# Kernel tuning notes

Hardware: AMD Instinct MI355X
Metric: run time of the kernel (lower is better)

Reference implementation:

```python
import jax, jax.numpy as jnp
import numpy as np

EPS = 1e-6

def setup_inputs() -> dict:
    key = jax.random.key(0)
    k1, k2 = jax.random.split(key)
    patch_feats = jax.random.normal(k1, (576, 768), dtype=jnp.float32)   # [N, D] ViT-B/16 @ 384 -> 24x24 patches
    memory = jax.random.normal(k2, (200000, 768), dtype=jnp.float32)     # [M, D] coreset memory bank
    return {"patch_feats": patch_feats, "memory": memory, "topk": 10}

def reference(patch_feats, memory, topk):
    # L2-normalize both sides (same eps placement as torch: x / (||x|| + eps))
    f = patch_feats / (jnp.linalg.norm(patch_feats, axis=1, keepdims=True) + EPS)  # [N, D]
    m = memory / (jnp.linalg.norm(memory, axis=1, keepdims=True) + EPS)            # [M, D]
    # cosine distance = 1 - sim; min over memory bank. Equivalent to the chunked
    # min-of-mins in the original (min is associative over chunks).
    sim = jnp.einsum('nd,md->nm', f, m)          # [N, M]
    patch_scores = jnp.min(1.0 - sim, axis=1)    # [N]
    # image score: mean of top-k patch scores
    k = min(topk, patch_scores.shape[0])
    topk_vals = jax.lax.top_k(patch_scores, k)[0]
    image_score = jnp.mean(topk_vals)
    return (patch_scores, image_score)
```

## Files before the change

kernel.cpp:

```cpp
#include <hip/hip_runtime.h>
#include <hip/hip_bf16.h>

#define DD 768
#define NPATCH 576
#define NPAD 640
#define NPT 40
#define BMR 64
#define QF 192
#define GRID 256
#define EPSF 1e-6f

typedef short bf16x8 __attribute__((ext_vector_type(8)));
typedef float f32x4 __attribute__((ext_vector_type(4)));

__device__ __forceinline__ unsigned short f2bf(float x) {
  __hip_bfloat16 h = __float2bfloat16(x);
  return __builtin_bit_cast(unsigned short, h);
}

__device__ __forceinline__ void gload_lds16(const float* g, char* lds) {
  __builtin_amdgcn_global_load_lds(
      (const __attribute__((address_space(1))) unsigned int*)(g),
      (__attribute__((address_space(3))) unsigned int*)(lds), 16, 0, 0);
}

__global__ __launch_bounds__(256) void k_norm(const float* __restrict__ pf,
                                              float* __restrict__ invn) {
  int row = blockIdx.x;
  int t = threadIdx.x;
  const float* src = pf + (size_t)row * DD;
  float v0 = src[t], v1 = src[t + 256], v2 = src[t + 512];
  float ss = v0 * v0 + v1 * v1 + v2 * v2;
#pragma unroll
  for (int m = 1; m < 64; m <<= 1) ss += __shfl_xor(ss, m, 64);
  __shared__ float wss[4];
  if ((t & 63) == 0) wss[t >> 6] = ss;
  __syncthreads();
  if (t == 0) {
    float tot = wss[0] + wss[1] + wss[2] + wss[3];
    invn[row] = 1.0f / (sqrtf(tot) + EPSF);
  }
}

__global__ __launch_bounds__(256) void k_pack(const float* __restrict__ pf,
                                              const float* __restrict__ invn,
                                              unsigned short* __restrict__ Fws) {
  int bid = blockIdx.x;
  int ks = bid / NPT, ptg = bid % NPT;
  int t = threadIdx.x;
  int i = t * 2;
  int s = i >> 3, j = i & 7;
  int p = ptg * 16 + (s & 15);
  int k = ks * 32 + (s >> 4) * 8 + j;
  unsigned int outw = 0;
  if (p < NPATCH) {
    float sc = invn[p];
    float a0 = pf[(size_t)p * DD + k] * sc;
    float a1 = pf[(size_t)p * DD + k + 1] * sc;
    outw = (unsigned int)f2bf(a0) | ((unsigned int)f2bf(a1) << 16);
  }
  ((unsigned int*)Fws)[(size_t)bid * 256 + t] = outw;
}

#define PACK_BW(bw, u0, u1)                                               \
  bw.x = (unsigned int)f2bf(u0.x) | ((unsigned int)f2bf(u0.y) << 16);     \
  bw.y = (unsigned int)f2bf(u0.z) | ((unsigned int)f2bf(u0.w) << 16);     \
  bw.z = (unsigned int)f2bf(u1.x) | ((unsigned int)f2bf(u1.y) << 16);     \
  bw.w = (unsigned int)f2bf(u1.z) | ((unsigned int)f2bf(u1.w) << 16);

#define SQ8(u0, u1)                                                        \
  (u0.x * u0.x + u0.y * u0.y + u0.z * u0.z + u0.w * u0.w +                 \
   u1.x * u1.x + u1.y * u1.y + u1.z * u1.z + u1.w * u1.w)

#define STEP(s)                                                              \
  {                                                                          \
    const unsigned short* Ak_ = Abase + (size_t)(q6 + (s)) * (NPT * 512);    \
    bf16x8 a_[5];                                                            \
    _Pragma("unroll") for (int p = 0; p < 5; ++p)                            \
        a_[p] = *(const bf16x8*)(Ak_ + p * 512);                             \
    __builtin_amdgcn_sched_barrier(0);                                       \
    gload_lds16((const float*)(gsrc + sbyte[s]),                             \
                (char*)BsF + dstb + (s) * 8192 + w * 1024);                  \
    __builtin_amdgcn_sched_barrier(0);                                       \
    _Pragma("unroll") for (int rt = 0; rt < 4; ++rt) {                       \
      int o0_ = rt * 12288 + rb768 + ((((s) * 8 + lhi2) ^ sw8x) << 4);       \
      float4 f0_ = *(const float4*)(bp + o0_);                               \
      float4 f1_ = *(const float4*)(bp + (o0_ ^ 16));                        \
      ssr[rt] += SQ8(f0_, f1_);                                              \
      uint4 bw_;                                                             \
      PACK_BW(bw_, f0_, f1_);                                                \
      bf16x8 b_ = __builtin_bit_cast(bf16x8, bw_);                           \
      _Pragma("unroll") for (int p = 0; p < 5; ++p)                          \
        acc[p][rt] = __builtin_amdgcn_mfma_f32_16x16x32_bf16(a_[p], b_, acc[p][rt], 0, 0, 0); \
    }                                                                        \
    __builtin_amdgcn_sched_barrier(0);                                       \
  }

__global__ __launch_bounds__(512, 2) void k_main(const unsigned short* __restrict__ Fws,
                                                 const float* __restrict__ mem,
                                                 float* __restrict__ partial,
                                                 int M, int nchunk) {
  __shared__ __align__(16) float BsF[2][12288];
  __shared__ float ssq[BMR];
  __shared__ float smin[NPAD];

  int t = threadIdx.x;
  int w = t >> 6, l = t & 63, l15 = l & 15, lhi = l >> 4;
  int lhi2 = lhi * 2, sw8x = l15 & 7, rb768 = l15 * 768;

  int sbyte[6];
#pragma unroll
  for (int i = 0; i < 6; ++i) {
    int idx = i * 512 + t;
    int r = idx / 48, sl = idx - r * 48;
    sbyte[i] = r * 3072 + ((sl ^ (r & 7)) << 4);
  }

  const unsigned short* Abase =
      Fws + (size_t)(w * 5) * 512 + (size_t)(lhi * 16 + l15) * 8;

  for (int i = t; i < NPAD; i += 512) smin[i] = 1e30f;

  int chunk = blockIdx.x;
  {
    const char* g0 = (const char*)mem + (size_t)chunk * (BMR * DD * 4);
#pragma unroll
    for (int i = 0; i < 6; ++i)
      gload_lds16((const float*)(g0 + sbyte[i]), (char*)BsF + i * 8192 + w * 1024);
  }

#pragma unroll 1
  for (; chunk < nchunk; chunk += GRID) {
    f32x4 acc[5][4];
#pragma unroll
    for (int p = 0; p < 5; ++p)
#pragma unroll
      for (int rt = 0; rt < 4; ++rt) {
        f32x4 z = {0.f, 0.f, 0.f, 0.f};
        acc[p][rt] = z;
      }
    float ssr[4] = {0.f, 0.f, 0.f, 0.f};

#pragma unroll 1
    for (int q = 0; q < 4; ++q) {
      __syncthreads();
      int qn = (q + 1) & 3;
      int chS = (q == 3) ? chunk + GRID : chunk;
      if (chS >= nchunk) chS = chunk;
      const char* gsrc = (const char*)mem +
          ((size_t)chS * (BMR * DD) + (size_t)qn * QF) * 4;
      int dstb = (qn & 1) * 49152;
      const char* bp = (const char*)BsF + (q & 1) * 49152;
      int q6 = q * 6;
      STEP(0) STEP(1) STEP(2) STEP(3) STEP(4) STEP(5)
    }

#pragma unroll
    for (int rt = 0; rt < 4; ++rt) {
      float v = ssr[rt];
      v += __shfl_xor(v, 16, 64);
      v += __shfl_xor(v, 32, 64);
      if (w == 0 && l < 16) ssq[rt * 16 + l15] = v;
    }
    __syncthreads();

    float inv_[4];
    bool okr[4];
#pragma unroll
    for (int rt = 0; rt < 4; ++rt) {
      inv_[rt] = 1.0f / (sqrtf(ssq[rt * 16 + l15]) + EPSF);
      okr[rt] = (chunk * BMR + rt * 16 + l15) < M;
    }
#pragma unroll
    for (int p = 0; p < 5; ++p) {
#pragma unroll
      for (int qq = 0; qq < 4; ++qq) {
        float d = okr[0] ? (1.0f - acc[p][0][qq] * inv_[0]) : 1e30f;
        d = fminf(d, okr[1] ? (1.0f - acc[p][1][qq] * inv_[1]) : 1e30f);
        d = fminf(d, okr[2] ? (1.0f - acc[p][2][qq] * inv_[2]) : 1e30f);
        d = fminf(d, okr[3] ? (1.0f - acc[p][3][qq] * inv_[3]) : 1e30f);
        d = fminf(d, __shfl_xor(d, 1, 64));
        d = fminf(d, __shfl_xor(d, 2, 64));
        d = fminf(d, __shfl_xor(d, 4, 64));
        d = fminf(d, __shfl_xor(d, 8, 64));
        if (l15 == 0) {
          int pl = (w * 5 + p) * 16 + lhi * 4 + qq;
          smin[pl] = fminf(smin[pl], d);
        }
      }
    }
  }

  __syncthreads();
  for (int i = t; i < NPATCH; i += 512)
    partial[(size_t)blockIdx.x * NPAD + i] = smin[i];
}

__global__ __launch_bounds__(256) void k_colmin(const float* __restrict__ partial,
                                                float* __restrict__ out, int nb) {
  int p = blockIdx.x;
  int t = threadIdx.x;
  float v = 1e30f;
  for (int b = t; b < nb; b += 256) v = fminf(v, partial[(size_t)b * NPAD + p]);
#pragma unroll
  for (int m = 1; m < 64; m <<= 1) v = fminf(v, __shfl_xor(v, m, 64));
  __shared__ float wmin[4];
  if ((t & 63) == 0) wmin[t >> 6] = v;
  __syncthreads();
  if (t == 0) out[p] = fminf(fminf(wmin[0], wmin[1]), fminf(wmin[2], wmin[3]));
}

__global__ __launch_bounds__(256) void k_topk(float* __restrict__ out,
                                              const int* __restrict__ topk_p) {
  __shared__ float vals[NPATCH];
  __shared__ float wv[4];
  __shared__ int wi[4];
  __shared__ float ssum;
  int t = threadIdx.x;
  for (int p = t; p < NPATCH; p += 256) vals[p] = out[p];
  if (t == 0) ssum = 0.f;
  int k = topk_p[0];
  if (k > NPATCH) k = NPATCH;
  if (k < 1) k = 1;
  __syncthreads();
  for (int it = 0; it < k; ++it) {
    float bv = -1e30f;
    int bi = 0;
    for (int p = t; p < NPATCH; p += 256) {
      float x = vals[p];
      if (x > bv) { bv = x; bi = p; }
    }
#pragma unroll
    for (int m = 1; m < 64; m <<= 1) {
      float ov = __shfl_xor(bv, m, 64);
      int oi = __shfl_xor(bi, m, 64);
      if (ov > bv || (ov == bv && oi < bi)) { bv = ov; bi = oi; }
    }
    if ((t & 63) == 0) { wv[t >> 6] = bv; wi[t >> 6] = bi; }
    __syncthreads();
    if (t == 0) {
      float fbv = wv[0]; int fbi = wi[0];
      for (int q = 1; q < 4; ++q)
        if (wv[q] > fbv || (wv[q] == fbv && wi[q] < fbi)) { fbv = wv[q]; fbi = wi[q]; }
      ssum += fbv;
      vals[fbi] = -1e30f;
    }
    __syncthreads();
  }
  if (t == 0) out[NPATCH] = ssum / (float)k;
}

extern "C" void kernel_launch(void* const* d_in, const int* in_sizes, int n_in,
                              void* d_out, int out_size, void* d_ws, size_t ws_size,
                              hipStream_t stream) {
  const float* pf = (const float*)d_in[0];
  const float* mem = (const float*)d_in[1];
  const int* topk = (const int*)d_in[2];
  float* out = (float*)d_out;
  int M = in_sizes[1] / DD;
  int nchunk = (M + BMR - 1) / BMR;

  unsigned short* Fws = (unsigned short*)d_ws;
  float* invn = (float*)((char*)d_ws + 983040);
  float* partial = (float*)((char*)d_ws + 983040 + 2560);

  int grid = GRID;
  if (grid > nchunk) grid = nchunk;

  k_norm<<<NPATCH, 256, 0, stream>>>(pf, invn);
  k_pack<<<24 * NPT, 256, 0, stream>>>(pf, invn, Fws);
  k_main<<<grid, 512, 0, stream>>>(Fws, mem, partial, M, nchunk);
  k_colmin<<<NPATCH, 256, 0, stream>>>(partial, out, grid);
  k_topk<<<1, 256, 0, stream>>>(out, topk);
}
```

Baseline: 421.4 us.

## Convert memory chunks to bf16 once in LDS via register-staged loads

Memory rows are now loaded from global into registers, converted to bf16 once per chunk, and written to LDS in halves. Before, each wave read raw fp32 from LDS and re-packed it to bf16 inside every MFMA step. A-operand fragments are double-buffered across steps, and the next half's global load is issued before the MFMA loop so it overlaps compute. The row-validity masks are removed by clamping out-of-range rows to M-1, which gives duplicate rows with identical distances instead of masked ones. Occupancy drops to one block per CU (launch_bounds 512,1), and a large register file (fL[12], two A buffers) is added.

```diff
diff --git a/kernel.cpp b/kernel.cpp
--- a/kernel.cpp
+++ b/kernel.cpp
@@ -6,7 +6,6 @@
 #define NPAD 640
 #define NPT 40
 #define BMR 64
-#define QF 192
 #define GRID 256
 #define EPSF 1e-6f
 
@@ -16,12 +15,6 @@
 __device__ __forceinline__ unsigned short f2bf(float x) {
   __hip_bfloat16 h = __float2bfloat16(x);
   return __builtin_bit_cast(unsigned short, h);
-}
-
-__device__ __forceinline__ void gload_lds16(const float* g, char* lds) {
-  __builtin_amdgcn_global_load_lds(
-      (const __attribute__((address_space(1))) unsigned int*)(g),
-      (__attribute__((address_space(3))) unsigned int*)(lds), 16, 0, 0);
 }
 
 __global__ __launch_bounds__(256) void k_norm(const float* __restrict__ pf,
@@ -72,61 +65,84 @@
   (u0.x * u0.x + u0.y * u0.y + u0.z * u0.z + u0.w * u0.w +                 \
    u1.x * u1.x + u1.y * u1.y + u1.z * u1.z + u1.w * u1.w)
 
-#define STEP(s)                                                              \
+#define GLOAD(cc, hp)                                                       \
+  {                                                                         \
+    int grow_ = (cc) * BMR + crow;                                          \
+    if (grow_ > M - 1) grow_ = M - 1;                                       \
+    const float* gp_ = mem + (size_t)grow_ * DD + (hp) * 384 + gcol;        \
+    _Pragma("unroll") for (int j = 0; j < 12; ++j)                          \
+        fL[j] = *(const float4*)(gp_ + j * 4);                              \
+  }
+
+#define CONV(hp)                                                            \
+  {                                                                         \
+    _Pragma("unroll") for (int j = 0; j < 6; ++j) {                         \
+      ssr += SQ8(fL[2 * j], fL[2 * j + 1]);                                 \
+      uint4 bw_;                                                            \
+      PACK_BW(bw_, fL[2 * j], fL[2 * j + 1]);                               \
+      *(uint4*)(BsB[hp] + wb[j]) = bw_;                                     \
+    }                                                                       \
+  }
+
+#define STEP(n, ARC, ARN)                                                    \
   {                                                                          \
-    const unsigned short* Ak_ = Abase + (size_t)(q6 + (s)) * (NPT * 512);    \
-    bf16x8 a_[5];                                                            \
+    const unsigned short* An_ = Abase + (size_t)(((n) + 1) % 24) * (NPT * 512); \
     _Pragma("unroll") for (int p = 0; p < 5; ++p)                            \
-        a_[p] = *(const bf16x8*)(Ak_ + p * 512);                             \
+        ARN[p] = *(const bf16x8*)(An_ + p * 512);                            \
     __builtin_amdgcn_sched_barrier(0);                                       \
-    gload_lds16((const float*)(gsrc + sbyte[s]),                             \
-                (char*)BsF + dstb + (s) * 8192 + w * 1024);                  \
+    const char* bp_ = BsB[(n) / 12];                                         \
+    int off_ = ((((n) % 12) * 4 + lhi) ^ fsw) << 4;                          \
+    bf16x8 b0_ = *(const bf16x8*)(bp_ + dsb[0] + off_);                      \
+    bf16x8 b1_ = *(const bf16x8*)(bp_ + dsb[1] + off_);                      \
+    bf16x8 b2_ = *(const bf16x8*)(bp_ + dsb[2] + off_);                      \
+    bf16x8 b3_ = *(const bf16x8*)(bp_ + dsb[3] + off_);                      \
+    asm volatile("s_waitcnt lgkmcnt(0)" ::: "memory");                       \
     __builtin_amdgcn_sched_barrier(0);                                       \
-    _Pragma("unroll") for (int rt = 0; rt < 4; ++rt) {                       \
-      int o0_ = rt * 12288 + rb768 + ((((s) * 8 + lhi2) ^ sw8x) << 4);       \
-      float4 f0_ = *(const float4*)(bp + o0_);                               \
-      float4 f1_ = *(const float4*)(bp + (o0_ ^ 16));                        \
-      ssr[rt] += SQ8(f0_, f1_);                                              \
-      uint4 bw_;                                                             \
-      PACK_BW(bw_, f0_, f1_);                                                \
-      bf16x8 b_ = __builtin_bit_cast(bf16x8, bw_);                           \
-      _Pragma("unroll") for (int p = 0; p < 5; ++p)                          \
-        acc[p][rt] = __builtin_amdgcn_mfma_f32_16x16x32_bf16(a_[p], b_, acc[p][rt], 0, 0, 0); \
+    _Pragma("unroll") for (int p = 0; p < 5; ++p) {                          \
+      acc[p][0] = __builtin_amdgcn_mfma_f32_16x16x32_bf16(ARC[p], b0_, acc[p][0], 0, 0, 0); \
+      acc[p][1] = __builtin_amdgcn_mfma_f32_16x16x32_bf16(ARC[p], b1_, acc[p][1], 0, 0, 0); \
+      acc[p][2] = __builtin_amdgcn_mfma_f32_16x16x32_bf16(ARC[p], b2_, acc[p][2], 0, 0, 0); \
+      acc[p][3] = __builtin_amdgcn_mfma_f32_16x16x32_bf16(ARC[p], b3_, acc[p][3], 0, 0, 0); \
     }                                                                        \
     __builtin_amdgcn_sched_barrier(0);                                       \
   }
 
-__global__ __launch_bounds__(512, 2) void k_main(const unsigned short* __restrict__ Fws,
+__global__ __launch_bounds__(512, 1) void k_main(const unsigned short* __restrict__ Fws,
                                                  const float* __restrict__ mem,
                                                  float* __restrict__ partial,
                                                  int M, int nchunk) {
-  __shared__ __align__(16) float BsF[2][12288];
+  __shared__ __align__(16) char BsB[2][49152];
   __shared__ float ssq[BMR];
   __shared__ float smin[NPAD];
 
   int t = threadIdx.x;
   int w = t >> 6, l = t & 63, l15 = l & 15, lhi = l >> 4;
-  int lhi2 = lhi * 2, sw8x = l15 & 7, rb768 = l15 * 768;
-
-  int sbyte[6];
-#pragma unroll
-  for (int i = 0; i < 6; ++i) {
-    int idx = i * 512 + t;
-    int r = idx / 48, sl = idx - r * 48;
-    sbyte[i] = r * 3072 + ((sl ^ (r & 7)) << 4);
-  }
+  int crow = t >> 3, c8 = t & 7;
+  int csw = crow & 7;
+  int gcol = c8 * 48;
+  int wb[6];
+#pragma unroll
+  for (int j = 0; j < 6; ++j) wb[j] = crow * 768 + (((c8 * 6 + j) ^ csw) << 4);
+  int fsw = l15 & 7;
+  int dsb[4];
+#pragma unroll
+  for (int rt = 0; rt < 4; ++rt) dsb[rt] = (rt * 16 + l15) * 768;
 
   const unsigned short* Abase =
       Fws + (size_t)(w * 5) * 512 + (size_t)(lhi * 16 + l15) * 8;
 
   for (int i = t; i < NPAD; i += 512) smin[i] = 1e30f;
+  __syncthreads();
+
+  float4 fL[12];
+  bf16x8 arE[5], arO[5];
 
   int chunk = blockIdx.x;
+  GLOAD(chunk, 0);
   {
-    const char* g0 = (const char*)mem + (size_t)chunk * (BMR * DD * 4);
-#pragma unroll
-    for (int i = 0; i < 6; ++i)
-      gload_lds16((const float*)(g0 + sbyte[i]), (char*)BsF + i * 8192 + w * 1024);
+    const unsigned short* A0 = Abase;
+#pragma unroll
+    for (int p = 0; p < 5; ++p) arE[p] = *(const bf16x8*)(A0 + p * 512);
   }
 
 #pragma unroll 1
@@ -139,52 +155,59 @@
         f32x4 z = {0.f, 0.f, 0.f, 0.f};
         acc[p][rt] = z;
       }
-    float ssr[4] = {0.f, 0.f, 0.f, 0.f};
-
-#pragma unroll 1
-    for (int q = 0; q < 4; ++q) {
-      __syncthreads();
-      int qn = (q + 1) & 3;
-      int chS = (q == 3) ? chunk + GRID : chunk;
-      if (chS >= nchunk) chS = chunk;
-      const char* gsrc = (const char*)mem +
-          ((size_t)chS * (BMR * DD) + (size_t)qn * QF) * 4;
-      int dstb = (qn & 1) * 49152;
-      const char* bp = (const char*)BsF + (q & 1) * 49152;
-      int q6 = q * 6;
-      STEP(0) STEP(1) STEP(2) STEP(3) STEP(4) STEP(5)
-    }
-
-#pragma unroll
-    for (int rt = 0; rt < 4; ++rt) {
-      float v = ssr[rt];
-      v += __shfl_xor(v, 16, 64);
-      v += __shfl_xor(v, 32, 64);
-      if (w == 0 && l < 16) ssq[rt * 16 + l15] = v;
-    }
-    __syncthreads();
+    float ssr = 0.f;
+
+    CONV(0);
+    asm volatile("s_waitcnt lgkmcnt(0)" ::: "memory");
+    __builtin_amdgcn_sched_barrier(0);
+    __builtin_amdgcn_s_barrier();
+    GLOAD(chunk, 1);
+    STEP(0, arE, arO)  STEP(1, arO, arE)  STEP(2, arE, arO)  STEP(3, arO, arE)
+    STEP(4, arE, arO)  STEP(5, arO, arE)  STEP(6, arE, arO)  STEP(7, arO, arE)
+    STEP(8, arE, arO)  STEP(9, arO, arE)  STEP(10, arE, arO) STEP(11, arO, arE)
+
+    CONV(1);
+    asm volatile("s_waitcnt lgkmcnt(0)" ::: "memory");
+    __builtin_amdgcn_sched_barrier(0);
+    __builtin_amdgcn_s_barrier();
+    {
+      int cn = chunk + GRID;
+      if (cn >= nchunk) cn = chunk;
+      GLOAD(cn, 0);
+    }
+    STEP(12, arE, arO) STEP(13, arO, arE) STEP(14, arE, arO) STEP(15, arO, arE)
+    STEP(16, arE, arO) STEP(17, arO, arE) STEP(18, arE, arO) STEP(19, arO, arE)
+    STEP(20, arE, arO) STEP(21, arO, arE) STEP(22, arE, arO) STEP(23, arO, arE)
+
+    {
+      float v = ssr;
+      v += __shfl_xor(v, 1, 64);
+      v += __shfl_xor(v, 2, 64);
+      v += __shfl_xor(v, 4, 64);
+      if (c8 == 0) ssq[crow] = v;
+    }
+    asm volatile("s_waitcnt lgkmcnt(0)" ::: "memory");
+    __builtin_amdgcn_sched_barrier(0);
+    __builtin_amdgcn_s_barrier();
 
     float inv_[4];
-    bool okr[4];
-#pragma unroll
-    for (int rt = 0; rt < 4; ++rt) {
+#pragma unroll
+    for (int rt = 0; rt < 4; ++rt)
       inv_[rt] = 1.0f / (sqrtf(ssq[rt * 16 + l15]) + EPSF);
-      okr[rt] = (chunk * BMR + rt * 16 + l15) < M;
-    }
 #pragma unroll
     for (int p = 0; p < 5; ++p) {
 #pragma unroll
-      for (int qq = 0; qq < 4; ++qq) {
-        float d = okr[0] ? (1.0f - acc[p][0][qq] * inv_[0]) : 1e30f;
-        d = fminf(d, okr[1] ? (1.0f - acc[p][1][qq] * inv_[1]) : 1e30f);
-        d = fminf(d, okr[2] ? (1.0f - acc[p][2][qq] * inv_[2]) : 1e30f);
-        d = fminf(d, okr[3] ? (1.0f - acc[p][3][qq] * inv_[3]) : 1e30f);
+      for (int q = 0; q < 4; ++q) {
+        float d = 1.0f - acc[p][0][q] * inv_[0];
+        d = fminf(d, 1.0f - acc[p][1][q] * inv_[1]);
+        d = fminf(d, 1.0f - acc[p][2][q] * inv_[2]);
+        d = fminf(d, 1.0f - acc[p][3][q] * inv_[3]);
         d = fminf(d, __shfl_xor(d, 1, 64));
         d = fminf(d, __shfl_xor(d, 2, 64));
         d = fminf(d, __shfl_xor(d, 4, 64));
         d = fminf(d, __shfl_xor(d, 8, 64));
         if (l15 == 0) {
-          int pl = (w * 5 + p) * 16 + lhi * 4 + qq;
+          int pl = (w * 5 + p) * 16 + lhi * 4 + q;
           smin[pl] = fminf(smin[pl], d);
         }
       }
```

Measured after the change: 1.140 ms. 171% more time.

## Convert memory tiles to bf16 once in LDS, then run MFMA from shared bf16 buffer

Applied to the files above, without the earlier changes.

Each fp32 memory-bank quarter-tile is now staged into LDS by global_load_lds, converted to bf16 once by all threads into a separate swizzled bf16 buffer, and computing squared norms happens during that conversion. Previously every wave redundantly converted the same B fragments. The MFMA phase then reads bf16 B fragments directly and register-caches the A fragments in groups of three k-steps. Prefetch uses explicit vmcnt/lgkmcnt waits with raw s_barrier, and priority is raised around the MFMA block. Occupancy drops to one 512-thread block per CU because LDS use grows. Out-of-range rows are now clamped to M-1 rather than masked, which gives duplicate rows instead of sentinel values.

```diff
diff --git a/kernel.cpp b/kernel.cpp
--- a/kernel.cpp
+++ b/kernel.cpp
@@ -6,7 +6,6 @@
 #define NPAD 640
 #define NPT 40
 #define BMR 64
-#define QF 192
 #define GRID 256
 #define EPSF 1e-6f
 
@@ -72,66 +71,117 @@
   (u0.x * u0.x + u0.y * u0.y + u0.z * u0.z + u0.w * u0.w +                 \
    u1.x * u1.x + u1.y * u1.y + u1.z * u1.z + u1.w * u1.w)
 
-#define STEP(s)                                                              \
-  {                                                                          \
-    const unsigned short* Ak_ = Abase + (size_t)(q6 + (s)) * (NPT * 512);    \
-    bf16x8 a_[5];                                                            \
-    _Pragma("unroll") for (int p = 0; p < 5; ++p)                            \
-        a_[p] = *(const bf16x8*)(Ak_ + p * 512);                             \
-    __builtin_amdgcn_sched_barrier(0);                                       \
-    gload_lds16((const float*)(gsrc + sbyte[s]),                             \
-                (char*)BsF + dstb + (s) * 8192 + w * 1024);                  \
-    __builtin_amdgcn_sched_barrier(0);                                       \
-    _Pragma("unroll") for (int rt = 0; rt < 4; ++rt) {                       \
-      int o0_ = rt * 12288 + rb768 + ((((s) * 8 + lhi2) ^ sw8x) << 4);       \
-      float4 f0_ = *(const float4*)(bp + o0_);                               \
-      float4 f1_ = *(const float4*)(bp + (o0_ ^ 16));                        \
-      ssr[rt] += SQ8(f0_, f1_);                                              \
-      uint4 bw_;                                                             \
-      PACK_BW(bw_, f0_, f1_);                                                \
-      bf16x8 b_ = __builtin_bit_cast(bf16x8, bw_);                           \
-      _Pragma("unroll") for (int p = 0; p < 5; ++p)                          \
-        acc[p][rt] = __builtin_amdgcn_mfma_f32_16x16x32_bf16(a_[p], b_, acc[p][rt], 0, 0, 0); \
-    }                                                                        \
-    __builtin_amdgcn_sched_barrier(0);                                       \
-  }
-
-__global__ __launch_bounds__(512, 2) void k_main(const unsigned short* __restrict__ Fws,
+#define ALOAD(ks0)                                                         \
+  { _Pragma("unroll") for (int s = 0; s < 3; ++s)                          \
+      _Pragma("unroll") for (int p = 0; p < 5; ++p)                        \
+        aR[s][p] = *(const bf16x8*)(Abase + (size_t)((ks0) + s) * (NPT * 512) + p * 512); \
+    __builtin_amdgcn_sched_barrier(0); }
+
+#define STAGEQ(cS, qS)                                                     \
+  { int cc_ = (cS);                                                        \
+    _Pragma("unroll") for (int i = 0; i < 6; ++i) {                        \
+      int gr_ = cc_ * BMR + srowL[i];                                      \
+      if (gr_ > Mm1) gr_ = Mm1;                                            \
+      gload_lds16((const float*)((const char*)mem + (size_t)gr_ * 3072 +   \
+                                 (qS) * 768 + scolb[i]),                   \
+                  (char*)fpq[(qS) & 1] + i * 8192 + w * 1024);             \
+    }                                                                      \
+    __builtin_amdgcn_sched_barrier(0); }
+
+#define CONVQ(bi)                                                          \
+  { const char* fb_ = fpq[bi];                                             \
+    _Pragma("unroll") for (int j = 0; j < 3; ++j) {                        \
+      float4 u0 = *(const float4*)(fb_ + cvr + (2 * c8 + 16 * j) * 16);    \
+      float4 u1 = *(const float4*)(fb_ + cvr + (2 * c8 + 16 * j) * 16 + 16); \
+      ssr += SQ8(u0, u1);                                                  \
+      uint4 bw_;                                                           \
+      PACK_BW(bw_, u0, u1);                                                \
+      *(uint4*)(bfq + cbw + wslb[j]) = bw_;                                \
+    } }
+
+#define STEPQ(s, as)                                                       \
+  { int off_ = (((s) * 4 + lhi) ^ fsw) << 4;                               \
+    bf16x8 b0_ = *(const bf16x8*)(bfq + dsb0 + off_);                      \
+    bf16x8 b1_ = *(const bf16x8*)(bfq + dsb1 + off_);                      \
+    bf16x8 b2_ = *(const bf16x8*)(bfq + dsb2 + off_);                      \
+    bf16x8 b3_ = *(const bf16x8*)(bfq + dsb3 + off_);                      \
+    asm volatile("s_waitcnt lgkmcnt(0)" ::: "memory");                     \
+    __builtin_amdgcn_sched_barrier(0);                                     \
+    __builtin_amdgcn_s_setprio(1);                                         \
+    _Pragma("unroll") for (int p = 0; p < 5; ++p) {                        \
+      acc[p][0] = __builtin_amdgcn_mfma_f32_16x16x32_bf16(aR[as][p], b0_, acc[p][0], 0, 0, 0); \
+      acc[p][1] = __builtin_amdgcn_mfma_f32_16x16x32_bf16(aR[as][p], b1_, acc[p][1], 0, 0, 0); \
+      acc[p][2] = __builtin_amdgcn_mfma_f32_16x16x32_bf16(aR[as][p], b2_, acc[p][2], 0, 0, 0); \
+      acc[p][3] = __builtin_amdgcn_mfma_f32_16x16x32_bf16(aR[as][p], b3_, acc[p][3], 0, 0, 0); \
+    }                                                                      \
+    __builtin_amdgcn_s_setprio(0);                                         \
+    __builtin_amdgcn_sched_barrier(0);                                     \
+  }
+
+#define PHASE(qq, cS, qS)                                                  \
+  {                                                                        \
+    ALOAD((qq) * 6)                                                        \
+    STAGEQ(cS, qS)                                                         \
+    asm volatile("s_waitcnt vmcnt(21)" ::: "memory");                      \
+    __builtin_amdgcn_sched_barrier(0);                                     \
+    __builtin_amdgcn_s_barrier();                                          \
+    CONVQ((qq) & 1)                                                        \
+    asm volatile("s_waitcnt lgkmcnt(0)" ::: "memory");                     \
+    __builtin_amdgcn_sched_barrier(0);                                     \
+    __builtin_amdgcn_s_barrier();                                          \
+    STEPQ(0, 0) STEPQ(1, 1) STEPQ(2, 2)                                    \
+    ALOAD((qq) * 6 + 3)                                                    \
+    STEPQ(3, 0) STEPQ(4, 1) STEPQ(5, 2)                                    \
+  }
+
+__global__ __launch_bounds__(512, 1) void k_main(const unsigned short* __restrict__ Fws,
                                                  const float* __restrict__ mem,
                                                  float* __restrict__ partial,
                                                  int M, int nchunk) {
-  __shared__ __align__(16) float BsF[2][12288];
+  __shared__ __align__(16) char fpq[2][49152];
+  __shared__ __align__(16) char bfq[24576];
   __shared__ float ssq[BMR];
   __shared__ float smin[NPAD];
 
   int t = threadIdx.x;
   int w = t >> 6, l = t & 63, l15 = l & 15, lhi = l >> 4;
-  int lhi2 = lhi * 2, sw8x = l15 & 7, rb768 = l15 * 768;
-
-  int sbyte[6];
+  int Mm1 = M - 1;
+
+  int srowL[6], scolb[6];
 #pragma unroll
   for (int i = 0; i < 6; ++i) {
-    int idx = i * 512 + t;
-    int r = idx / 48, sl = idx - r * 48;
-    sbyte[i] = r * 3072 + ((sl ^ (r & 7)) << 4);
-  }
+    int flat = i * 512 + t;
+    int r = flat / 48;
+    srowL[i] = r;
+    scolb[i] = (flat - r * 48) * 16;
+  }
+  int crow = t >> 3, c8 = t & 7;
+  int cvr = crow * 768, cbw = crow * 384, csw = crow & 7;
+  int wslb[3];
+#pragma unroll
+  for (int j = 0; j < 3; ++j) wslb[j] = ((c8 + 8 * j) ^ csw) << 4;
+  int fsw = l15 & 7;
+  int dsb0 = (0 * 16 + l15) * 384;
+  int dsb1 = (1 * 16 + l15) * 384;
+  int dsb2 = (2 * 16 + l15) * 384;
+  int dsb3 = (3 * 16 + l15) * 384;
 
   const unsigned short* Abase =
       Fws + (size_t)(w * 5) * 512 + (size_t)(lhi * 16 + l15) * 8;
 
   for (int i = t; i < NPAD; i += 512) smin[i] = 1e30f;
 
+  bf16x8 aR[3][5];
+  f32x4 acc[5][4];
+
   int chunk = blockIdx.x;
-  {
-    const char* g0 = (const char*)mem + (size_t)chunk * (BMR * DD * 4);
-#pragma unroll
-    for (int i = 0; i < 6; ++i)
-      gload_lds16((const float*)(g0 + sbyte[i]), (char*)BsF + i * 8192 + w * 1024);
-  }
+  STAGEQ(chunk, 0)
 
 #pragma unroll 1
   for (; chunk < nchunk; chunk += GRID) {
-    f32x4 acc[5][4];
+    int cnx = chunk + GRID;
+    if (cnx >= nchunk) cnx = chunk;
+
 #pragma unroll
     for (int p = 0; p < 5; ++p)
 #pragma unroll
@@ -139,52 +189,42 @@
         f32x4 z = {0.f, 0.f, 0.f, 0.f};
         acc[p][rt] = z;
       }
-    float ssr[4] = {0.f, 0.f, 0.f, 0.f};
-
-#pragma unroll 1
-    for (int q = 0; q < 4; ++q) {
-      __syncthreads();
-      int qn = (q + 1) & 3;
-      int chS = (q == 3) ? chunk + GRID : chunk;
-      if (chS >= nchunk) chS = chunk;
-      const char* gsrc = (const char*)mem +
-          ((size_t)chS * (BMR * DD) + (size_t)qn * QF) * 4;
-      int dstb = (qn & 1) * 49152;
-      const char* bp = (const char*)BsF + (q & 1) * 49152;
-      int q6 = q * 6;
-      STEP(0) STEP(1) STEP(2) STEP(3) STEP(4) STEP(5)
-    }
-
-#pragma unroll
-    for (int rt = 0; rt < 4; ++rt) {
-      float v = ssr[rt];
-      v += __shfl_xor(v, 16, 64);
-      v += __shfl_xor(v, 32, 64);
-      if (w == 0 && l < 16) ssq[rt * 16 + l15] = v;
-    }
-    __syncthreads();
-
-    float inv_[4];
-    bool okr[4];
-#pragma unroll
-    for (int rt = 0; rt < 4; ++rt) {
-      inv_[rt] = 1.0f / (sqrtf(ssq[rt * 16 + l15]) + EPSF);
-      okr[rt] = (chunk * BMR + rt * 16 + l15) < M;
-    }
+    float ssr = 0.f;
+
+    PHASE(0, chunk, 1)
+    PHASE(1, chunk, 2)
+    PHASE(2, chunk, 3)
+    PHASE(3, cnx, 0)
+
+    {
+      float v = ssr;
+      v += __shfl_xor(v, 1, 64);
+      v += __shfl_xor(v, 2, 64);
+      v += __shfl_xor(v, 4, 64);
+      if (c8 == 0) ssq[crow] = v;
+    }
+    asm volatile("s_waitcnt lgkmcnt(0)" ::: "memory");
+    __builtin_amdgcn_sched_barrier(0);
+    __builtin_amdgcn_s_barrier();
+
+    float inv0 = 1.0f / (sqrtf(ssq[l15]) + EPSF);
+    float inv1 = 1.0f / (sqrtf(ssq[16 + l15]) + EPSF);
+    float inv2 = 1.0f / (sqrtf(ssq[32 + l15]) + EPSF);
+    float inv3 = 1.0f / (sqrtf(ssq[48 + l15]) + EPSF);
 #pragma unroll
     for (int p = 0; p < 5; ++p) {
 #pragma unroll
-      for (int qq = 0; qq < 4; ++qq) {
-        float d = okr[0] ? (1.0f - acc[p][0][qq] * inv_[0]) : 1e30f;
-        d = fminf(d, okr[1] ? (1.0f - acc[p][1][qq] * inv_[1]) : 1e30f);
-        d = fminf(d, okr[2] ? (1.0f - acc[p][2][qq] * inv_[2]) : 1e30f);
-        d = fminf(d, okr[3] ? (1.0f - acc[p][3][qq] * inv_[3]) : 1e30f);
+      for (int q = 0; q < 4; ++q) {
+        float d = 1.0f - acc[p][0][q] * inv0;
+        d = fminf(d, 1.0f - acc[p][1][q] * inv1);
+        d = fminf(d, 1.0f - acc[p][2][q] * inv2);
+        d = fminf(d, 1.0f - acc[p][3][q] * inv3);
         d = fminf(d, __shfl_xor(d, 1, 64));
         d = fminf(d, __shfl_xor(d, 2, 64));
         d = fminf(d, __shfl_xor(d, 4, 64));
         d = fminf(d, __shfl_xor(d, 8, 64));
         if (l15 == 0) {
-          int pl = (w * 5 + p) * 16 + lhi * 4 + qq;
+          int pl = (w * 5 + p) * 16 + lhi * 4 + q;
           smin[pl] = fminf(smin[pl], d);
         }
       }
```

New measurement: 1.074 ms. 2.55x slower.
